# Kernel optimization log

Measured on AMD Instinct MI355X. Metric: run time of the kernel, lower is better.

## Reference

```python
import jax, jax.numpy as jnp
import numpy as np

EMBED_DIM = 1024
NUM_HEADS = 16
HEAD_DIM = EMBED_DIM // NUM_HEADS
SEQ = 2048
BATCH = 2


def setup_inputs() -> dict:
    key = jax.random.key(0)
    ks = jax.random.split(key, 8)
    s = 1.0 / np.sqrt(EMBED_DIM)
    return {
        "query": jax.random.normal(ks[0], (SEQ, BATCH, EMBED_DIM), jnp.float32),
        "key": jax.random.normal(ks[1], (SEQ, BATCH, EMBED_DIM), jnp.float32),
        "value": jax.random.normal(ks[2], (SEQ, BATCH, EMBED_DIM), jnp.float32),
        "Wq": jax.random.normal(ks[3], (EMBED_DIM, EMBED_DIM), jnp.float32) * s,
        "Wk": jax.random.normal(ks[4], (EMBED_DIM, EMBED_DIM), jnp.float32) * s,
        "Wv": jax.random.normal(ks[5], (EMBED_DIM, EMBED_DIM), jnp.float32) * s,
        "in_bias": jnp.zeros((3 * EMBED_DIM,), jnp.float32),
        "Wo": jax.random.normal(ks[6], (EMBED_DIM, EMBED_DIM), jnp.float32) * s,
        "bo": jnp.zeros((EMBED_DIM,), jnp.float32),
    }


def reference(query, key, value, Wq, Wk, Wv, in_bias, Wo, bo):
    E, H, D = EMBED_DIM, NUM_HEADS, HEAD_DIM
    # seq-first -> batch-first: [T,B,E] -> [B,T,E]
    q_in = jnp.transpose(query, (1, 0, 2))
    k_in = jnp.transpose(key, (1, 0, 2))
    v_in = jnp.transpose(value, (1, 0, 2))
    B, T, _ = q_in.shape

    # fused in-projection (torch _in_projection: x @ W.T + b)
    q = q_in @ Wq.T + in_bias[:E]
    k = k_in @ Wk.T + in_bias[E:2 * E]
    v = v_in @ Wv.T + in_bias[2 * E:]

    # split heads: [B,T,E] -> [B,H,T,D]
    def split_heads(x):
        return jnp.transpose(x.reshape(B, T, H, D), (0, 2, 1, 3))

    q, k, v = split_heads(q), split_heads(k), split_heads(v)

    # multi-linear (causal linear) attention with outer-product KV state:
    # kv_store[b,h,t] = sum_{s<=t} k_s (outer) v_s        -> [B,H,T,D,D]
    kv_store = jnp.cumsum(jnp.einsum("bhtk,bhtv->bhtkv", k, v), axis=2)
    scale = 1.0 / np.sqrt(D)
    attn = jnp.einsum("bhtk,bhtkv->bhtv", q, kv_store) * scale  # [B,H,T,D]

    # merge heads + out projection
    out = jnp.transpose(attn, (0, 2, 1, 3)).reshape(B, T, E)
    out = out @ Wo.T + bo
    # batch-first -> seq-first
    return jnp.transpose(out, (1, 0, 2))
```

## Files before the change

### kernel.cpp

```cpp
#include <hip/hip_runtime.h>


#define TSEQ 2048
#define BBATCH 2
#define EE 1024
#define TOK 4096
#define NCH 32

typedef _Float16 half8 __attribute__((ext_vector_type(8)));
typedef _Float16 half4 __attribute__((ext_vector_type(4)));
typedef float f32x4 __attribute__((ext_vector_type(4)));

#ifndef __has_builtin
#define __has_builtin(x) 0
#endif
#if __has_builtin(__builtin_amdgcn_global_load_lds)
#define USE_GLL 1
#endif

#ifdef USE_GLL
typedef __attribute__((address_space(1))) const unsigned int guint_t;
typedef __attribute__((address_space(3))) unsigned int luint_t;
#endif

__global__ __launch_bounds__(256) void pack_x_kernel(
    const float* __restrict__ q, const float* __restrict__ k,
    const float* __restrict__ v,
    _Float16* __restrict__ xq, _Float16* __restrict__ xk,
    _Float16* __restrict__ xv) {
  const int blk = blockIdx.x;
  const int m = blk >> 12;
  const int row = blk & 4095;
  const int b = row >> 11, t = row & 2047;
  const float* src = (m == 0 ? q : (m == 1 ? k : v)) +
                     (size_t)t * (BBATCH * EE) + (size_t)b * EE;
  _Float16* dst = (m == 0 ? xq : (m == 1 ? xk : xv)) + (size_t)row * EE;
  const int e = threadIdx.x * 4;
  f32x4 f = *(const f32x4*)&src[e];
  half4 h;
  h[0] = (_Float16)f[0]; h[1] = (_Float16)f[1];
  h[2] = (_Float16)f[2]; h[3] = (_Float16)f[3];
  *(half4*)&dst[e] = h;
}

__global__ __launch_bounds__(256) void pack_w_kernel(
    const float* __restrict__ wq, const float* __restrict__ wk,
    const float* __restrict__ wv, const float* __restrict__ wo,
    _Float16* __restrict__ wb) {
  const int blk = blockIdx.x;
  const int m = blk >> 10, row = blk & 1023;
  const float* src =
      (m == 0 ? wq : (m == 1 ? wk : (m == 2 ? wv : wo))) + (size_t)row * EE;
  _Float16* dst = wb + (size_t)m * EE * EE + (size_t)row * EE;
  const int e = threadIdx.x * 4;
  f32x4 f = *(const f32x4*)&src[e];
  half4 h;
  h[0] = (_Float16)f[0]; h[1] = (_Float16)f[1];
  h[2] = (_Float16)f[2]; h[3] = (_Float16)f[3];
  *(half4*)&dst[e] = h;
}

template <int MODE>
__global__ __launch_bounds__(256) void gemm_nt(
    const _Float16* __restrict__ A, const _Float16* __restrict__ Bm,
    const float* __restrict__ bias, _Float16* __restrict__ O0,
    _Float16* __restrict__ O1, float* __restrict__ OF) {
  __shared__ __align__(16) _Float16 Abuf[128 * 64];
  __shared__ __align__(16) _Float16 Bbuf[128 * 64];
  const int tid = threadIdx.x;
  const int lane = tid & 63, w = tid >> 6;
  const int wr = w >> 1, wc = w & 1;
  const int l15 = lane & 15, lg = lane >> 4;
  const long arow0 = (long)blockIdx.y * 128;
  const long brow0 = (long)blockIdx.x * 128;

  f32x4 acc[4][4] = {};

  for (int kt = 0; kt < 16; ++kt) {
    const int k0 = kt * 64;
    __syncthreads();
#pragma unroll
    for (int i = 0; i < 4; ++i) {
      const int flat = i * 256 + tid;
      const int r = flat >> 3, c = (flat & 7) * 8;
      const _Float16* ga = &A[(size_t)(arow0 + r) * 1024 + k0 + c];
      const _Float16* gb = &Bm[(size_t)(brow0 + r) * 1024 + k0 + c];
#ifdef USE_GLL
      const int ubase = (i * 256 + w * 64) * 8;
      __builtin_amdgcn_global_load_lds((guint_t*)ga, (luint_t*)&Abuf[ubase],
                                       16, 0, 0);
      __builtin_amdgcn_global_load_lds((guint_t*)gb, (luint_t*)&Bbuf[ubase],
                                       16, 0, 0);
#else
      *(half8*)&Abuf[flat * 8] = *(const half8*)ga;
      *(half8*)&Bbuf[flat * 8] = *(const half8*)gb;
#endif
    }
    __syncthreads();
#pragma unroll
    for (int ks = 0; ks < 2; ++ks) {
      half8 af[4], bf[4];
#pragma unroll
      for (int mi = 0; mi < 4; ++mi)
        af[mi] = *(const half8*)&Abuf[(wr * 64 + mi * 16 + l15) * 64 +
                                      ks * 32 + lg * 8];
#pragma unroll
      for (int ni = 0; ni < 4; ++ni)
        bf[ni] = *(const half8*)&Bbuf[(wc * 64 + ni * 16 + l15) * 64 +
                                      ks * 32 + lg * 8];
#pragma unroll
      for (int mi = 0; mi < 4; ++mi)
#pragma unroll
        for (int ni = 0; ni < 4; ++ni)
          acc[mi][ni] = __builtin_amdgcn_mfma_f32_16x16x32_f16(
              af[mi], bf[ni], acc[mi][ni], 0, 0, 0);
    }
  }

#pragma unroll
  for (int mi = 0; mi < 4; ++mi) {
#pragma unroll
    for (int ni = 0; ni < 4; ++ni) {
      const int mloc = wr * 64 + mi * 16 + lg * 4;
      const int nloc = wc * 64 + ni * 16 + l15;
      const long gm = arow0 + mloc;
      const long gn = brow0 + nloc;
      if (MODE == 3) {
        const int t = (int)(gn & 2047), b2 = (int)(gn >> 11);
        f32x4 res;
#pragma unroll
        for (int r = 0; r < 4; ++r) res[r] = acc[mi][ni][r] + bias[gm + r];
        *(f32x4*)&OF[(size_t)t * (BBATCH * EE) + (size_t)b2 * EE + gm] = res;
      } else {
        const float bv = bias[gn];
        float vv[4];
#pragma unroll
        for (int r = 0; r < 4; ++r) vv[r] = acc[mi][ni][r] + bv;
        if (MODE == 0 || MODE == 1) {
#pragma unroll
          for (int r = 0; r < 4; ++r)
            O0[(size_t)(gm + r) * 1024 + gn] = (_Float16)vv[r];
        }
        if (MODE == 1 || MODE == 2) {
          half4 pk;
#pragma unroll
          for (int r = 0; r < 4; ++r) pk[r] = (_Float16)vv[r];
          *(half4*)&O1[(size_t)gn * TOK + gm] = pk;
        }
      }
    }
  }
}

__global__ __launch_bounds__(64) void chunk_g_kernel(
    const _Float16* __restrict__ KT, const _Float16* __restrict__ VT,
    _Float16* __restrict__ GT) {
  const int c = blockIdx.x & 31, bh = blockIdx.x >> 5;
  const int b = bh >> 4, h = bh & 15;
  const int lane = threadIdx.x, l15 = lane & 15, lg = lane >> 4;
  const long tok0 = (long)b * TSEQ + c * 64;

  half8 af[4][2], bf[4][2];
#pragma unroll
  for (int ma = 0; ma < 4; ++ma)
#pragma unroll
    for (int ks = 0; ks < 2; ++ks) {
      const size_t rowoff = (size_t)(h * 64 + ma * 16 + l15) * TOK + tok0 +
                            ks * 32 + lg * 8;
      af[ma][ks] = *(const half8*)&KT[rowoff];
      bf[ma][ks] = *(const half8*)&VT[rowoff];
    }
  f32x4 acc[4][4] = {};
#pragma unroll
  for (int ks = 0; ks < 2; ++ks)
#pragma unroll
    for (int ma = 0; ma < 4; ++ma)
#pragma unroll
      for (int nb = 0; nb < 4; ++nb)
        acc[ma][nb] = __builtin_amdgcn_mfma_f32_16x16x32_f16(
            af[ma][ks], bf[nb][ks], acc[ma][nb], 0, 0, 0);
  _Float16* g = GT + ((size_t)bh * NCH + c) * 4096;
#pragma unroll
  for (int ma = 0; ma < 4; ++ma)
#pragma unroll
    for (int nb = 0; nb < 4; ++nb) {
      half4 pk;
#pragma unroll
      for (int r = 0; r < 4; ++r) pk[r] = (_Float16)acc[ma][nb][r];
      *(half4*)&g[(nb * 16 + l15) * 64 + ma * 16 + lg * 4] = pk;
    }
}

__global__ __launch_bounds__(256) void scan_kernel(
    const _Float16* __restrict__ GT, _Float16* __restrict__ ST) {
  const int gid = blockIdx.x * 256 + threadIdx.x;
  const int bh = gid >> 12, el = gid & 4095;
  const size_t base = (size_t)bh * NCH * 4096 + el;
  float acc = 0.f;
  for (int c = 0; c < NCH; ++c) {
    ST[base + (size_t)c * 4096] = (_Float16)acc;
    acc += (float)GT[base + (size_t)c * 4096];
  }
}

__global__ __launch_bounds__(64) void attn_chunk_kernel(
    const _Float16* __restrict__ Q, const _Float16* __restrict__ Kb,
    const _Float16* __restrict__ VT, const _Float16* __restrict__ ST,
    _Float16* __restrict__ attn) {
  __shared__ __align__(16) _Float16 sc[64 * 72];
  const int c = blockIdx.x & 31, bh = blockIdx.x >> 5;
  const int b = bh >> 4, h = bh & 15;
  const int lane = threadIdx.x, l15 = lane & 15, lg = lane >> 4;
  const long tok0 = (long)b * TSEQ + c * 64;

  half8 qb[4][2];
#pragma unroll
  for (int nb = 0; nb < 4; ++nb)
#pragma unroll
    for (int ks = 0; ks < 2; ++ks)
      qb[nb][ks] = *(const half8*)&Q[(size_t)(tok0 + nb * 16 + l15) * EE +
                                     h * 64 + ks * 32 + lg * 8];

  f32x4 sT[4][4] = {};
#pragma unroll
  for (int ks = 0; ks < 2; ++ks) {
    half8 kf[4];
#pragma unroll
    for (int ma = 0; ma < 4; ++ma)
      kf[ma] = *(const half8*)&Kb[(size_t)(tok0 + ma * 16 + l15) * EE +
                                  h * 64 + ks * 32 + lg * 8];
#pragma unroll
    for (int ma = 0; ma < 4; ++ma)
#pragma unroll
      for (int nb = 0; nb < 4; ++nb)
        sT[ma][nb] = __builtin_amdgcn_mfma_f32_16x16x32_f16(
            kf[ma], qb[nb][ks], sT[ma][nb], 0, 0, 0);
  }
#pragma unroll
  for (int ma = 0; ma < 4; ++ma)
#pragma unroll
    for (int nb = 0; nb < 4; ++nb) {
      const int tp0 = ma * 16 + lg * 4, t = nb * 16 + l15;
      half4 pk;
#pragma unroll
      for (int r = 0; r < 4; ++r)
        pk[r] = (tp0 + r <= t) ? (_Float16)sT[ma][nb][r] : (_Float16)0.f;
      *(half4*)&sc[t * 72 + tp0] = pk;
    }
  __syncthreads();

  f32x4 o[4][4] = {};
  const _Float16* st = ST + ((size_t)bh * NCH + c) * 4096;
#pragma unroll
  for (int ks = 0; ks < 2; ++ks) {
    half8 sf[4];
#pragma unroll
    for (int ma = 0; ma < 4; ++ma)
      sf[ma] = *(const half8*)&st[(ma * 16 + l15) * 64 + ks * 32 + lg * 8];
#pragma unroll
    for (int ma = 0; ma < 4; ++ma)
#pragma unroll
      for (int nb = 0; nb < 4; ++nb)
        o[ma][nb] = __builtin_amdgcn_mfma_f32_16x16x32_f16(
            sf[ma], qb[nb][ks], o[ma][nb], 0, 0, 0);
  }
#pragma unroll
  for (int ks = 0; ks < 2; ++ks) {
    half8 vf[4], sb[4];
#pragma unroll
    for (int ma = 0; ma < 4; ++ma)
      vf[ma] = *(const half8*)&VT[(size_t)(h * 64 + ma * 16 + l15) * TOK +
                                  tok0 + ks * 32 + lg * 8];
#pragma unroll
    for (int nb = 0; nb < 4; ++nb)
      sb[nb] = *(const half8*)&sc[(nb * 16 + l15) * 72 + ks * 32 + lg * 8];
#pragma unroll
    for (int ma = 0; ma < 4; ++ma)
#pragma unroll
      for (int nb = 0; nb < 4; ++nb)
        o[ma][nb] = __builtin_amdgcn_mfma_f32_16x16x32_f16(
            vf[ma], sb[nb], o[ma][nb], 0, 0, 0);
  }
#pragma unroll
  for (int ma = 0; ma < 4; ++ma)
#pragma unroll
    for (int nb = 0; nb < 4; ++nb) {
      const int t = nb * 16 + l15, d20 = ma * 16 + lg * 4;
      half4 pk;
#pragma unroll
      for (int r = 0; r < 4; ++r) pk[r] = (_Float16)(o[ma][nb][r] * 0.125f);
      *(half4*)&attn[(size_t)(tok0 + t) * EE + h * 64 + d20] = pk;
    }
}

extern "C" void kernel_launch(void* const* d_in, const int* in_sizes, int n_in,
                              void* d_out, int out_size, void* d_ws,
                              size_t ws_size, hipStream_t stream) {
  const float* q = (const float*)d_in[0];
  const float* k = (const float*)d_in[1];
  const float* v = (const float*)d_in[2];
  const float* Wq = (const float*)d_in[3];
  const float* Wk = (const float*)d_in[4];
  const float* Wv = (const float*)d_in[5];
  const float* in_bias = (const float*)d_in[6];
  const float* Wo = (const float*)d_in[7];
  const float* bo = (const float*)d_in[8];
  float* out = (float*)d_out;

  char* ws = (char*)d_ws;
  const size_t MB = 1u << 20;
  _Float16* wb = (_Float16*)(ws + 0 * MB);
  _Float16* xq = (_Float16*)(ws + 8 * MB);
  _Float16* xk = (_Float16*)(ws + 16 * MB);
  _Float16* xv = (_Float16*)(ws + 24 * MB);
  _Float16* Qb = (_Float16*)(ws + 32 * MB);
  _Float16* Kbf = (_Float16*)(ws + 40 * MB);
  _Float16* KT = (_Float16*)(ws + 48 * MB);
  _Float16* VT = (_Float16*)(ws + 56 * MB);
  _Float16* attnb = (_Float16*)(ws + 8 * MB);
  _Float16* GT = (_Float16*)(ws + 16 * MB);
  _Float16* STb = (_Float16*)(ws + 24 * MB);

  pack_x_kernel<<<12288, 256, 0, stream>>>(q, k, v, xq, xk, xv);
  pack_w_kernel<<<4096, 256, 0, stream>>>(Wq, Wk, Wv, Wo, wb);

  dim3 gp(8, 32);
  gemm_nt<0><<<gp, 256, 0, stream>>>(xq, wb, in_bias, Qb, nullptr, nullptr);
  gemm_nt<1><<<gp, 256, 0, stream>>>(xk, wb + 1048576, in_bias + 1024, Kbf,
                                     KT, nullptr);
  gemm_nt<2><<<gp, 256, 0, stream>>>(xv, wb + 2097152, in_bias + 2048,
                                     nullptr, VT, nullptr);

  chunk_g_kernel<<<1024, 64, 0, stream>>>(KT, VT, GT);
  scan_kernel<<<512, 256, 0, stream>>>(GT, STb);
  attn_chunk_kernel<<<1024, 64, 0, stream>>>(Qb, Kbf, VT, STb, attnb);

  dim3 go(32, 8);
  gemm_nt<3><<<go, 256, 0, stream>>>(wb + 3145728, attnb, bo, nullptr,
                                     nullptr, out);
}
```

Before: 237.1 us.

## Double-buffer GEMM LDS tiles and merge three in-projection GEMMs into one launch

Restructures the fp16 MFMA GEMM core to double-buffer LDS tiles, issuing async global-to-LDS loads for the next k-tile before computing the current one and waiting with a partial vmcnt. The Q, K and V in-projections are also fused into a single launch with a 3x wider grid, selecting inputs and epilogue by block index. This aims to hide global load latency and fill the GPU better than three separate small launches. LDS use per block doubles, which can reduce occupancy.

```diff
diff --git a/kernel.cpp b/kernel.cpp
--- a/kernel.cpp
+++ b/kernel.cpp
@@ -60,54 +60,61 @@
   *(half4*)&dst[e] = h;
 }
 
-template <int MODE>
-__global__ __launch_bounds__(256) void gemm_nt(
+__device__ __forceinline__ void stage_tile(
     const _Float16* __restrict__ A, const _Float16* __restrict__ Bm,
-    const float* __restrict__ bias, _Float16* __restrict__ O0,
-    _Float16* __restrict__ O1, float* __restrict__ OF) {
-  __shared__ __align__(16) _Float16 Abuf[128 * 64];
-  __shared__ __align__(16) _Float16 Bbuf[128 * 64];
-  const int tid = threadIdx.x;
+    long arow0, long brow0, int k0, int tid, int w,
+    _Float16* __restrict__ Ab, _Float16* __restrict__ Bb) {
+#pragma unroll
+  for (int i = 0; i < 4; ++i) {
+    const int flat = i * 256 + tid;
+    const int r = flat >> 3, c = (flat & 7) * 8;
+    const _Float16* ga = &A[(size_t)(arow0 + r) * 1024 + k0 + c];
+    const _Float16* gb = &Bm[(size_t)(brow0 + r) * 1024 + k0 + c];
+#ifdef USE_GLL
+    const int ubase = (i * 256 + w * 64) * 8;
+    __builtin_amdgcn_global_load_lds((guint_t*)ga, (luint_t*)&Ab[ubase], 16, 0,
+                                     0);
+    __builtin_amdgcn_global_load_lds((guint_t*)gb, (luint_t*)&Bb[ubase], 16, 0,
+                                     0);
+#else
+    *(half8*)&Ab[flat * 8] = *(const half8*)ga;
+    *(half8*)&Bb[flat * 8] = *(const half8*)gb;
+#endif
+  }
+}
+
+__device__ __forceinline__ void gemm_core(
+    const _Float16* __restrict__ A, const _Float16* __restrict__ Bm,
+    long arow0, long brow0, int tid, f32x4 (&acc)[4][4],
+    _Float16 (&Ab)[2][8192], _Float16 (&Bb)[2][8192]) {
   const int lane = tid & 63, w = tid >> 6;
   const int wr = w >> 1, wc = w & 1;
   const int l15 = lane & 15, lg = lane >> 4;
-  const long arow0 = (long)blockIdx.y * 128;
-  const long brow0 = (long)blockIdx.x * 128;
-
-  f32x4 acc[4][4] = {};
-
+
+#ifdef USE_GLL
+  stage_tile(A, Bm, arow0, brow0, 0, tid, w, Ab[0], Bb[0]);
   for (int kt = 0; kt < 16; ++kt) {
-    const int k0 = kt * 64;
-    __syncthreads();
-#pragma unroll
-    for (int i = 0; i < 4; ++i) {
-      const int flat = i * 256 + tid;
-      const int r = flat >> 3, c = (flat & 7) * 8;
-      const _Float16* ga = &A[(size_t)(arow0 + r) * 1024 + k0 + c];
-      const _Float16* gb = &Bm[(size_t)(brow0 + r) * 1024 + k0 + c];
-#ifdef USE_GLL
-      const int ubase = (i * 256 + w * 64) * 8;
-      __builtin_amdgcn_global_load_lds((guint_t*)ga, (luint_t*)&Abuf[ubase],
-                                       16, 0, 0);
-      __builtin_amdgcn_global_load_lds((guint_t*)gb, (luint_t*)&Bbuf[ubase],
-                                       16, 0, 0);
-#else
-      *(half8*)&Abuf[flat * 8] = *(const half8*)ga;
-      *(half8*)&Bbuf[flat * 8] = *(const half8*)gb;
-#endif
-    }
-    __syncthreads();
+    const int cur = kt & 1;
+    if (kt < 15) {
+      stage_tile(A, Bm, arow0, brow0, (kt + 1) * 64, tid, w, Ab[cur ^ 1],
+                 Bb[cur ^ 1]);
+      asm volatile("s_waitcnt vmcnt(8)" ::: "memory");
+    } else {
+      asm volatile("s_waitcnt vmcnt(0)" ::: "memory");
+    }
+    __builtin_amdgcn_s_barrier();
+    asm volatile("" ::: "memory");
 #pragma unroll
     for (int ks = 0; ks < 2; ++ks) {
       half8 af[4], bf[4];
 #pragma unroll
       for (int mi = 0; mi < 4; ++mi)
-        af[mi] = *(const half8*)&Abuf[(wr * 64 + mi * 16 + l15) * 64 +
-                                      ks * 32 + lg * 8];
+        af[mi] = *(const half8*)&Ab[cur][(wr * 64 + mi * 16 + l15) * 64 +
+                                         ks * 32 + lg * 8];
 #pragma unroll
       for (int ni = 0; ni < 4; ++ni)
-        bf[ni] = *(const half8*)&Bbuf[(wc * 64 + ni * 16 + l15) * 64 +
-                                      ks * 32 + lg * 8];
+        bf[ni] = *(const half8*)&Bb[cur][(wc * 64 + ni * 16 + l15) * 64 +
+                                         ks * 32 + lg * 8];
 #pragma unroll
       for (int mi = 0; mi < 4; ++mi)
 #pragma unroll
@@ -115,39 +122,115 @@
           acc[mi][ni] = __builtin_amdgcn_mfma_f32_16x16x32_f16(
               af[mi], bf[ni], acc[mi][ni], 0, 0, 0);
     }
-  }
-
+    asm volatile("" ::: "memory");
+    __builtin_amdgcn_s_barrier();
+  }
+#else
+  for (int kt = 0; kt < 16; ++kt) {
+    __syncthreads();
+    stage_tile(A, Bm, arow0, brow0, kt * 64, tid, w, Ab[0], Bb[0]);
+    __syncthreads();
+#pragma unroll
+    for (int ks = 0; ks < 2; ++ks) {
+      half8 af[4], bf[4];
+#pragma unroll
+      for (int mi = 0; mi < 4; ++mi)
+        af[mi] = *(const half8*)&Ab[0][(wr * 64 + mi * 16 + l15) * 64 +
+                                       ks * 32 + lg * 8];
+#pragma unroll
+      for (int ni = 0; ni < 4; ++ni)
+        bf[ni] = *(const half8*)&Bb[0][(wc * 64 + ni * 16 + l15) * 64 +
+                                       ks * 32 + lg * 8];
+#pragma unroll
+      for (int mi = 0; mi < 4; ++mi)
+#pragma unroll
+        for (int ni = 0; ni < 4; ++ni)
+          acc[mi][ni] = __builtin_amdgcn_mfma_f32_16x16x32_f16(
+              af[mi], bf[ni], acc[mi][ni], 0, 0, 0);
+    }
+  }
+#endif
+}
+
+__global__ __launch_bounds__(256) void gemm_inproj(
+    const _Float16* __restrict__ X, const _Float16* __restrict__ WB,
+    const float* __restrict__ bias, _Float16* __restrict__ Qb,
+    _Float16* __restrict__ Kbf, _Float16* __restrict__ KT,
+    _Float16* __restrict__ VT) {
+  __shared__ __align__(16) _Float16 Ab[2][8192];
+  __shared__ __align__(16) _Float16 Bb[2][8192];
+  const int tid = threadIdx.x;
+  const int which = blockIdx.x >> 3;
+  const long arow0 = (long)blockIdx.y * 128;
+  const long brow0 = (long)(blockIdx.x & 7) * 128;
+  const _Float16* A = X + (size_t)which * (TOK * EE);
+  const _Float16* Bm = WB + (size_t)which * (EE * EE);
+  const float* bs = bias + which * EE;
+
+  f32x4 acc[4][4] = {};
+  gemm_core(A, Bm, arow0, brow0, tid, acc, Ab, Bb);
+
+  const int lane = tid & 63, w = tid >> 6;
+  const int wr = w >> 1, wc = w & 1;
+  const int l15 = lane & 15, lg = lane >> 4;
 #pragma unroll
   for (int mi = 0; mi < 4; ++mi) {
 #pragma unroll
     for (int ni = 0; ni < 4; ++ni) {
-      const int mloc = wr * 64 + mi * 16 + lg * 4;
-      const int nloc = wc * 64 + ni * 16 + l15;
-      const long gm = arow0 + mloc;
-      const long gn = brow0 + nloc;
-      if (MODE == 3) {
-        const int t = (int)(gn & 2047), b2 = (int)(gn >> 11);
-        f32x4 res;
-#pragma unroll
-        for (int r = 0; r < 4; ++r) res[r] = acc[mi][ni][r] + bias[gm + r];
-        *(f32x4*)&OF[(size_t)t * (BBATCH * EE) + (size_t)b2 * EE + gm] = res;
+      const long gm = arow0 + wr * 64 + mi * 16 + lg * 4;
+      const long gn = brow0 + wc * 64 + ni * 16 + l15;
+      const float bv = bs[gn];
+      float vv[4];
+#pragma unroll
+      for (int r = 0; r < 4; ++r) vv[r] = acc[mi][ni][r] + bv;
+      if (which == 0) {
+#pragma unroll
+        for (int r = 0; r < 4; ++r)
+          Qb[(size_t)(gm + r) * EE + gn] = (_Float16)vv[r];
+      } else if (which == 1) {
+#pragma unroll
+        for (int r = 0; r < 4; ++r)
+          Kbf[(size_t)(gm + r) * EE + gn] = (_Float16)vv[r];
+        half4 pk;
+#pragma unroll
+        for (int r = 0; r < 4; ++r) pk[r] = (_Float16)vv[r];
+        *(half4*)&KT[(size_t)gn * TOK + gm] = pk;
       } else {
-        const float bv = bias[gn];
-        float vv[4];
-#pragma unroll
-        for (int r = 0; r < 4; ++r) vv[r] = acc[mi][ni][r] + bv;
-        if (MODE == 0 || MODE == 1) {
-#pragma unroll
-          for (int r = 0; r < 4; ++r)
-            O0[(size_t)(gm + r) * 1024 + gn] = (_Float16)vv[r];
-        }
-        if (MODE == 1 || MODE == 2) {
-          half4 pk;
-#pragma unroll
-          for (int r = 0; r < 4; ++r) pk[r] = (_Float16)vv[r];
-          *(half4*)&O1[(size_t)gn * TOK + gm] = pk;
-        }
+        half4 pk;
+#pragma unroll
+        for (int r = 0; r < 4; ++r) pk[r] = (_Float16)vv[r];
+        *(half4*)&VT[(size_t)gn * TOK + gm] = pk;
       }
+    }
+  }
+}
+
+__global__ __launch_bounds__(256) void gemm_out(
+    const _Float16* __restrict__ Wo, const _Float16* __restrict__ ATT,
+    const float* __restrict__ bo, float* __restrict__ OF) {
+  __shared__ __align__(16) _Float16 Ab[2][8192];
+  __shared__ __align__(16) _Float16 Bb[2][8192];
+  const int tid = threadIdx.x;
+  const long arow0 = (long)blockIdx.y * 128;
+  const long brow0 = (long)blockIdx.x * 128;
+
+  f32x4 acc[4][4] = {};
+  gemm_core(Wo, ATT, arow0, brow0, tid, acc, Ab, Bb);
+
+  const int lane = tid & 63, w = tid >> 6;
+  const int wr = w >> 1, wc = w & 1;
+  const int l15 = lane & 15, lg = lane >> 4;
+#pragma unroll
+  for (int mi = 0; mi < 4; ++mi) {
+#pragma unroll
+    for (int ni = 0; ni < 4; ++ni) {
+      const long gm = arow0 + wr * 64 + mi * 16 + lg * 4;
+      const long gn = brow0 + wc * 64 + ni * 16 + l15;
+      const int t = (int)(gn & 2047), b2 = (int)(gn >> 11);
+      f32x4 res;
+#pragma unroll
+      for (int r = 0; r < 4; ++r) res[r] = acc[mi][ni][r] + bo[gm + r];
+      *(f32x4*)&OF[(size_t)t * (BBATCH * EE) + (size_t)b2 * EE + gm] = res;
     }
   }
 }
@@ -324,18 +407,13 @@
   pack_x_kernel<<<12288, 256, 0, stream>>>(q, k, v, xq, xk, xv);
   pack_w_kernel<<<4096, 256, 0, stream>>>(Wq, Wk, Wv, Wo, wb);
 
-  dim3 gp(8, 32);
-  gemm_nt<0><<<gp, 256, 0, stream>>>(xq, wb, in_bias, Qb, nullptr, nullptr);
-  gemm_nt<1><<<gp, 256, 0, stream>>>(xk, wb + 1048576, in_bias + 1024, Kbf,
-                                     KT, nullptr);
-  gemm_nt<2><<<gp, 256, 0, stream>>>(xv, wb + 2097152, in_bias + 2048,
-                                     nullptr, VT, nullptr);
+  dim3 gi(24, 32);
+  gemm_inproj<<<gi, 256, 0, stream>>>(xq, wb, in_bias, Qb, Kbf, KT, VT);
 
   chunk_g_kernel<<<1024, 64, 0, stream>>>(KT, VT, GT);
   scan_kernel<<<512, 256, 0, stream>>>(GT, STb);
   attn_chunk_kernel<<<1024, 64, 0, stream>>>(Qb, Kbf, VT, STb, attnb);
 
   dim3 go(32, 8);
-  gemm_nt<3><<<go, 256, 0, stream>>>(wb + 3145728, attnb, bo, nullptr,
-                                     nullptr, out);
-}
+  gemm_out<<<go, 256, 0, stream>>>(wb + 3145728, attnb, bo, out);
+}
```

After: 220.7 us. 6.9% less time.
